# Kernel optimization log

Hardware: AMD Instinct MI355X
Metric: run time of the kernel (lower is better)

## Reference

```python
import jax, jax.numpy as jnp
import numpy as np

B, S, D, H, HD, I = 8, 512, 2048, 32, 64, 8192
REL = 2 * 512 - 1  # 1023
EPS = 1e-6
SCALE = float(np.sqrt(HD))


def _layernorm(x, g, b):
    mu = jnp.mean(x, axis=-1, keepdims=True)
    var = jnp.mean(jnp.square(x - mu), axis=-1, keepdims=True)
    return (x - mu) / jnp.sqrt(var + EPS) * g + b


def setup_inputs() -> dict:
    key = jax.random.key(0)
    ks = jax.random.split(key, 10)
    s = 0.02
    return {
        "hidden_states": jax.random.normal(ks[0], (B, S, D), dtype=jnp.float32),
        "wq": jax.random.normal(ks[1], (D, D), dtype=jnp.float32) * s,
        "wk": jax.random.normal(ks[2], (D, D), dtype=jnp.float32) * s,
        "wv": jax.random.normal(ks[3], (D, D), dtype=jnp.float32) * s,
        "wo": jax.random.normal(ks[4], (D, D), dtype=jnp.float32) * s,
        "rel_pos": jax.random.normal(ks[5], (REL, HD), dtype=jnp.float32),
        "ln1_g": jnp.ones((D,), jnp.float32),
        "ln1_b": jnp.zeros((D,), jnp.float32),
        "gate_w": jax.random.normal(ks[6], (D, I), dtype=jnp.float32) * s,
        "up_w": jax.random.normal(ks[7], (D, I), dtype=jnp.float32) * s,
        "down_w": jax.random.normal(ks[8], (I, D), dtype=jnp.float32) * s,
        "ln2_g": jnp.ones((D,), jnp.float32),
        "ln2_b": jnp.zeros((D,), jnp.float32),
    }


def reference(hidden_states, wq, wk, wv, wo, rel_pos, ln1_g, ln1_b,
              gate_w, up_w, down_w, ln2_g, ln2_b):
    x = hidden_states
    # --- MultiHeadAttentionXL ---
    q = (x @ wq).reshape(B, S, H, HD)
    k = (x @ wk).reshape(B, S, H, HD)
    v = (x @ wv).reshape(B, S, H, HD)
    scores = jnp.einsum('bqhd,bkhd->bhqk', q, k) / SCALE
    # relative position bias (seq_len <= 512 path)
    pos = jnp.arange(S)
    rp = jnp.clip(pos[None, :] - pos[:, None] + 512 - 1, 0, REL - 1)  # [S,S]
    bias = rel_pos[rp].mean(axis=-1)  # [S,S]
    scores = scores + bias[None, None]
    attn = jax.nn.softmax(scores, axis=-1)
    ctx = jnp.einsum('bhqk,bkhd->bqhd', attn, v).reshape(B, S, D)
    attn_out = ctx @ wo
    # residual + post-LN
    h = _layernorm(x + attn_out, ln1_g, ln1_b)
    # --- FeedForwardXL (SwiGLU) ---
    gate = jax.nn.silu(h @ gate_w)
    up = h @ up_w
    ffn = (gate * up) @ down_w
    h = _layernorm(h + ffn, ln2_g, ln2_b)
    return h
```

## Files before the change

kernel.cpp:

```cpp
#include <hip/hip_runtime.h>
#include <cstdint>
#include <cstddef>

typedef _Float16 f16;
typedef _Float16 f16x8 __attribute__((ext_vector_type(8)));
typedef _Float16 f16x4 __attribute__((ext_vector_type(4)));
typedef _Float16 f16x2 __attribute__((ext_vector_type(2)));
typedef float    f32x4 __attribute__((ext_vector_type(4)));

constexpr int S_ = 512, D_ = 2048, H_ = 32, HD_ = 64, I_ = 8192;
constexpr int M_ = 4096;

enum { OP_F32 = 0, OP_F16 = 1, OP_SILU = 2, OP_QKT = 3, OP_PV = 4,
       OP_QKV = 6, OP_UPG = 7, OP_RES = 8 };

__device__ __forceinline__ void gl_lds16(const void* g, void* lds) {
  __builtin_amdgcn_global_load_lds(
      (const __attribute__((address_space(1))) void*)g,
      (__attribute__((address_space(3))) void*)lds, 16, 0, 0);
}

template <int BM, int BN, int WR, int WC, int OP, bool BF32>
__global__ __launch_bounds__(256, 2) void gemm_k(
    const f16* __restrict__ A, int lda,
    const void* __restrict__ Bv, int ldb,
    void* __restrict__ Cp, int ldc,
    int K, int bh0, const float* __restrict__ relmean,
    const void* __restrict__ Bv2, const void* __restrict__ Bv3) {
  constexpr int BK = 32;
  constexpr int WM = BM / WR, WN = BN / WC;
  constexpr int IM = WM / 16, IN = WN / 16;
  constexpr int CA = BM / 64, CB = BN / 64;
  __shared__ __align__(16) f16 As[BM * BK];
  __shared__ __align__(16) f16 Bs[BN * BK];
  const int tid = threadIdx.x, wave = tid >> 6, lane = tid & 63;
  const int wm = wave / WC, wn = wave % WC;
  const int bn = blockIdx.x, bm = blockIdx.y, bz = blockIdx.z;

  long aoff = 0, boff = 0;
  if constexpr (OP == OP_QKT) {
    int bh = bh0 + bz;
    long hb = (long)(bh >> 5) * (S_ * D_) + (long)(bh & (H_ - 1)) * HD_;
    aoff = hb; boff = hb;
  }
  if constexpr (OP == OP_PV) {
    int bh = bh0 + bz;
    aoff = (long)bz * S_ * S_;
    boff = (long)bh * HD_ * S_;
  }

  const f16* Ab = A + aoff + (long)bm * BM * lda;
  const f16* Bb = nullptr;
  const float* Bf = nullptr;
  if constexpr (BF32) {
    const float* base = (const float*)Bv;
    if constexpr (OP == OP_QKV)
      base = (bz == 0) ? (const float*)Bv : (bz == 1) ? (const float*)Bv2
                                                      : (const float*)Bv3;
    Bf = base + (long)bn * BN;
  } else {
    Bb = (const f16*)Bv + boff + (long)bn * BN * ldb;
  }

  f32x4 acc[IM][IN];
#pragma unroll
  for (int i = 0; i < IM; i++)
#pragma unroll
    for (int j = 0; j < IN; j++) acc[i][j] = {0.f, 0.f, 0.f, 0.f};

  const int lr = lane >> 2, l4 = lane & 3;
  const int q8 = (lane >> 4) * 8, l15 = lane & 15;
  constexpr int NG = BN / 4;
  constexpr int KPT = BN / 32;
  const int ng = tid & (NG - 1), kg = tid / NG;

  for (int kt = 0; kt < K; kt += BK) {
#pragma unroll
    for (int c = 0; c < CA; c++) {
      int reg = wave * CA + c;
      int row = reg * 16 + lr;
      gl_lds16(Ab + (long)row * lda + kt + l4 * 8, &As[reg * 512]);
    }
    if constexpr (!BF32) {
#pragma unroll
      for (int c = 0; c < CB; c++) {
        int reg = wave * CB + c;
        int row = reg * 16 + lr;
        gl_lds16(Bb + (long)row * ldb + kt + l4 * 8, &Bs[reg * 512]);
      }
    } else {
      f32x4 v[KPT];
#pragma unroll
      for (int i2 = 0; i2 < KPT; i2++)
        v[i2] = *(const f32x4*)&Bf[(long)(kt + kg * KPT + i2) * ldb + ng * 4];
#pragma unroll
      for (int j2 = 0; j2 < 4; j2++) {
        int n = ng * 4 + j2;
        int k0 = (kg * KPT) ^ ((ng & 3) * 8);
        if constexpr (KPT == 4) {
          f16x4 w = {(f16)v[0][j2], (f16)v[1][j2], (f16)v[2][j2], (f16)v[3][j2]};
          *(f16x4*)&Bs[n * BK + k0] = w;
        } else {
          f16x2 w = {(f16)v[0][j2], (f16)v[1][j2]};
          *(f16x2*)&Bs[n * BK + k0] = w;
        }
      }
    }
    __syncthreads();
    f16x8 af[IM], bfr[IN];
#pragma unroll
    for (int i = 0; i < IM; i++)
      af[i] = *(const f16x8*)&As[(wm * WM + i * 16 + l15) * BK + q8];
#pragma unroll
    for (int j = 0; j < IN; j++) {
      int colL = wn * WN + j * 16 + l15;
      int koff = BF32 ? (q8 ^ (((colL >> 2) & 3) * 8)) : q8;
      bfr[j] = *(const f16x8*)&Bs[colL * BK + koff];
    }
#pragma unroll
    for (int i = 0; i < IM; i++)
#pragma unroll
      for (int j = 0; j < IN; j++)
        acc[i][j] = __builtin_amdgcn_mfma_f32_16x16x32_f16(af[i], bfr[j], acc[i][j], 0, 0, 0);
    __syncthreads();
  }

  const int r0 = bm * BM + wm * WM + (lane >> 4) * 4;
  const int c0 = bn * BN + wn * WN + l15;
#pragma unroll
  for (int i = 0; i < IM; i++) {
#pragma unroll
    for (int j = 0; j < IN; j++) {
      int rowb = r0 + i * 16;
      int col = c0 + j * 16;
      if constexpr (OP == OP_F32) {
        float* C = (float*)Cp;
#pragma unroll
        for (int t = 0; t < 4; t++) C[(long)(rowb + t) * ldc + col] = acc[i][j][t];
      } else if constexpr (OP == OP_F16) {
        f16* C = (f16*)Cp;
#pragma unroll
        for (int t = 0; t < 4; t++) C[(long)(rowb + t) * ldc + col] = (f16)acc[i][j][t];
      } else if constexpr (OP == OP_SILU) {
        f16* C = (f16*)Cp;
#pragma unroll
        for (int t = 0; t < 4; t++) {
          float v = acc[i][j][t];
          C[(long)(rowb + t) * ldc + col] = (f16)(v / (1.f + __expf(-v)));
        }
      } else if constexpr (OP == OP_UPG) {
        f16* C = (f16*)Cp;
        const f16* G = (const f16*)Bv2;
#pragma unroll
        for (int t = 0; t < 4; t++) {
          long idx = (long)(rowb + t) * ldc + col;
          C[idx] = (f16)((float)G[idx] * acc[i][j][t]);
        }
      } else if constexpr (OP == OP_RES) {
        f16* C = (f16*)Cp;
#pragma unroll
        for (int t = 0; t < 4; t++) {
          long idx = (long)(rowb + t) * ldc + col;
          C[idx] = (f16)(acc[i][j][t] + relmean[idx]);
        }
      } else if constexpr (OP == OP_QKT) {
        f16* C = (f16*)Cp + (long)bz * S_ * S_;
#pragma unroll
        for (int t = 0; t < 4; t++) {
          int r = rowb + t;
          C[(long)r * S_ + col] = (f16)(acc[i][j][t] * 0.125f + relmean[col - r + 511]);
        }
      } else if constexpr (OP == OP_PV) {
        int bh = bh0 + bz;
        f16* C = (f16*)Cp + (long)(bh >> 5) * (S_ * D_) + (long)(bh & (H_ - 1)) * HD_;
#pragma unroll
        for (int t = 0; t < 4; t++) C[(long)(rowb + t) * ldc + col] = (f16)acc[i][j][t];
      } else if constexpr (OP == OP_QKV) {
        f16* C = (f16*)Cp;
        if (bz < 2) {
          f16* Cq = C + (long)bz * M_ * D_;
#pragma unroll
          for (int t = 0; t < 4; t++) Cq[(long)(rowb + t) * ldc + col] = (f16)acc[i][j][t];
        } else {
          f16* Cv = C + (long)2 * M_ * D_;
          int b = rowb >> 9, s0 = rowb & 511, h = col >> 6, hd = col & 63;
          f16x4 pk;
#pragma unroll
          for (int t = 0; t < 4; t++) pk[t] = (f16)acc[i][j][t];
          *(f16x4*)&Cv[((long)(b * H_ + h) * HD_ + hd) * S_ + s0] = pk;
        }
      }
    }
  }
}

__global__ void cvt_f16_k(const float* __restrict__ in, f16* __restrict__ out, int n4) {
  int i = blockIdx.x * 256 + threadIdx.x;
  if (i >= n4) return;
  f32x4 v = ((const f32x4*)in)[i];
  f16x4 o;
#pragma unroll
  for (int t = 0; t < 4; t++) o[t] = (f16)v[t];
  ((f16x4*)out)[i] = o;
}

__global__ void relmean_k(const float* __restrict__ rel, float* __restrict__ rm) {
  int i = blockIdx.x * 256 + threadIdx.x;
  if (i >= 1023) return;
  float s = 0.f;
#pragma unroll 8
  for (int d = 0; d < 64; d++) s += rel[i * 64 + d];
  rm[i] = s * (1.f / 64.f);
}

__global__ __launch_bounds__(256) void softmax_k(f16* __restrict__ Sc) {
  int r = blockIdx.x * 4 + (threadIdx.x >> 6);
  int lane = threadIdx.x & 63;
  f16* s = Sc + (long)r * S_;
  f16x8 d = *(const f16x8*)&s[lane * 8];
  float v[8], mx = -1e30f;
#pragma unroll
  for (int i = 0; i < 8; i++) { v[i] = (float)d[i]; mx = fmaxf(mx, v[i]); }
  for (int off = 32; off; off >>= 1) mx = fmaxf(mx, __shfl_xor(mx, off));
  float sum = 0.f;
#pragma unroll
  for (int i = 0; i < 8; i++) { v[i] = __expf(v[i] - mx); sum += v[i]; }
  for (int off = 32; off; off >>= 1) sum += __shfl_xor(sum, off);
  float rs = 1.f / sum;
  f16x8 o;
#pragma unroll
  for (int i = 0; i < 8; i++) o[i] = (f16)(v[i] * rs);
  *(f16x8*)&s[lane * 8] = o;
}

__global__ __launch_bounds__(256) void ln_k(const float* __restrict__ X,
                                            const float* __restrict__ Y,
                                            const float* __restrict__ g,
                                            const float* __restrict__ b,
                                            float* __restrict__ outF,
                                            f16* __restrict__ outH) {
  int row = blockIdx.x;
  const float* x = X + (long)row * D_;
  const float* y = Y + (long)row * D_;
  int t = threadIdx.x;
  float v[8], sum = 0.f, sq = 0.f;
#pragma unroll
  for (int i = 0; i < 8; i++) {
    int idx = t + i * 256;
    float val = x[idx] + y[idx];
    v[i] = val; sum += val; sq += val * val;
  }
  for (int off = 32; off; off >>= 1) { sum += __shfl_down(sum, off); sq += __shfl_down(sq, off); }
  __shared__ float s1[4], s2[4];
  if ((t & 63) == 0) { s1[t >> 6] = sum; s2[t >> 6] = sq; }
  __syncthreads();
  sum = s1[0] + s1[1] + s1[2] + s1[3];
  sq = s2[0] + s2[1] + s2[2] + s2[3];
  float mu = sum * (1.f / D_);
  float rstd = rsqrtf(sq * (1.f / D_) - mu * mu + 1e-6f);
#pragma unroll
  for (int i = 0; i < 8; i++) {
    int idx = t + i * 256;
    float nv = (v[i] - mu) * rstd * g[idx] + b[idx];
    outF[(long)row * D_ + idx] = nv;
    outH[(long)row * D_ + idx] = (f16)nv;
  }
}

__global__ __launch_bounds__(256) void ln2s_k(const f16* __restrict__ X,
                                              const float* __restrict__ g,
                                              const float* __restrict__ b,
                                              float* __restrict__ outF) {
  int row = blockIdx.x;
  const f16* x = X + (long)row * D_;
  int t = threadIdx.x;
  float v[8], sum = 0.f, sq = 0.f;
#pragma unroll
  for (int i = 0; i < 8; i++) {
    float val = (float)x[t + i * 256];
    v[i] = val; sum += val; sq += val * val;
  }
  for (int off = 32; off; off >>= 1) { sum += __shfl_down(sum, off); sq += __shfl_down(sq, off); }
  __shared__ float s1[4], s2[4];
  if ((t & 63) == 0) { s1[t >> 6] = sum; s2[t >> 6] = sq; }
  __syncthreads();
  sum = s1[0] + s1[1] + s1[2] + s1[3];
  sq = s2[0] + s2[1] + s2[2] + s2[3];
  float mu = sum * (1.f / D_);
  float rstd = rsqrtf(sq * (1.f / D_) - mu * mu + 1e-6f);
#pragma unroll
  for (int i = 0; i < 8; i++) {
    int idx = t + i * 256;
    outF[(long)row * D_ + idx] = (v[i] - mu) * rstd * g[idx] + b[idx];
  }
}

extern "C" void kernel_launch(void* const* d_in, const int* in_sizes, int n_in,
                              void* d_out, int out_size, void* d_ws, size_t ws_size,
                              hipStream_t stream) {
  const float* x    = (const float*)d_in[0];
  const float* wq   = (const float*)d_in[1];
  const float* wk   = (const float*)d_in[2];
  const float* wv   = (const float*)d_in[3];
  const float* wo   = (const float*)d_in[4];
  const float* rel  = (const float*)d_in[5];
  const float* ln1g = (const float*)d_in[6];
  const float* ln1b = (const float*)d_in[7];
  const float* gw   = (const float*)d_in[8];
  const float* uw   = (const float*)d_in[9];
  const float* dw   = (const float*)d_in[10];
  const float* ln2g = (const float*)d_in[11];
  const float* ln2b = (const float*)d_in[12];
  float* out = (float*)d_out;

  constexpr size_t MD2 = (size_t)M_ * D_ * 2;
  if (ws_size < 8 * MD2 + 4096) return;
  char* w = (char*)d_ws;
  f16* qb  = (f16*)(w + 0 * MD2);
  f16* vT  = (f16*)(w + 2 * MD2);
  f16* xb  = (f16*)(w + 3 * MD2);
  f16* sc  = (f16*)(w + 4 * MD2);
  f16* h1h = (f16*)(w + 6 * MD2);
  float* relmean = (float*)(w + 8 * MD2);
  f16* ctxb = xb;
  float* attn_out = (float*)qb;
  float* h1 = (float*)sc;
  f16* gc = qb;
  f16* h2h = h1h;

  cvt_f16_k<<<M_ * D_ / 4 / 256, 256, 0, stream>>>(x, xb, M_ * D_ / 4);
  relmean_k<<<4, 256, 0, stream>>>(rel, relmean);

  gemm_k<128, 128, 2, 2, OP_QKV, true><<<dim3(16, 32, 3), 256, 0, stream>>>(
      xb, D_, wq, D_, qb, D_, D_, 0, nullptr, wk, wv);

  for (int c = 0; c < 4; c++) {
    int bh0 = c * 64;
    gemm_k<128, 128, 2, 2, OP_QKT, false><<<dim3(4, 4, 64), 256, 0, stream>>>(
        qb, D_, qb + (size_t)M_ * D_, D_, sc, S_, HD_, bh0, relmean, nullptr, nullptr);
    softmax_k<<<64 * S_ / 4, 256, 0, stream>>>(sc);
    gemm_k<64, 64, 2, 2, OP_PV, false><<<dim3(1, 8, 64), 256, 0, stream>>>(
        sc, S_, vT, S_, ctxb, D_, S_, bh0, nullptr, nullptr, nullptr);
  }

  gemm_k<128, 64, 2, 2, OP_F32, true><<<dim3(32, 32, 1), 256, 0, stream>>>(
      ctxb, D_, wo, D_, attn_out, D_, D_, 0, nullptr, nullptr, nullptr);
  ln_k<<<M_, 256, 0, stream>>>(x, attn_out, ln1g, ln1b, h1, h1h);

  gemm_k<128, 128, 2, 2, OP_SILU, true><<<dim3(64, 32, 1), 256, 0, stream>>>(
      h1h, D_, gw, I_, gc, I_, D_, 0, nullptr, nullptr, nullptr);
  gemm_k<128, 128, 2, 2, OP_UPG, true><<<dim3(64, 32, 1), 256, 0, stream>>>(
      h1h, D_, uw, I_, gc, I_, D_, 0, nullptr, gc, nullptr);
  gemm_k<128, 64, 2, 2, OP_RES, true><<<dim3(32, 32, 1), 256, 0, stream>>>(
      gc, I_, dw, D_, h2h, D_, I_, 0, h1, nullptr, nullptr);
  ln2s_k<<<M_, 256, 0, stream>>>(h2h, ln2g, ln2b, out);
}
```

Baseline: 1.306 ms.

## Pre-transpose weights to f16, fuse gate/up GEMM, split FFN into halves

```diff
diff --git a/kernel.cpp b/kernel.cpp
--- a/kernel.cpp
+++ b/kernel.cpp
@@ -5,14 +5,13 @@
 typedef _Float16 f16;
 typedef _Float16 f16x8 __attribute__((ext_vector_type(8)));
 typedef _Float16 f16x4 __attribute__((ext_vector_type(4)));
-typedef _Float16 f16x2 __attribute__((ext_vector_type(2)));
 typedef float    f32x4 __attribute__((ext_vector_type(4)));
 
 constexpr int S_ = 512, D_ = 2048, H_ = 32, HD_ = 64, I_ = 8192;
 constexpr int M_ = 4096;
-
-enum { OP_F32 = 0, OP_F16 = 1, OP_SILU = 2, OP_QKT = 3, OP_PV = 4,
-       OP_QKV = 6, OP_UPG = 7, OP_RES = 8 };
+constexpr int IH_ = 4096;
+
+enum { OP_F32 = 0, OP_QKT = 3, OP_PV = 4, OP_QKV = 6, OP_GU = 9, OP_ADD = 10 };
 
 __device__ __forceinline__ void gl_lds16(const void* g, void* lds) {
   __builtin_amdgcn_global_load_lds(
@@ -20,19 +19,20 @@
       (__attribute__((address_space(3))) void*)lds, 16, 0, 0);
 }
 
-template <int BM, int BN, int WR, int WC, int OP, bool BF32>
+template <int BM, int BN, int WR, int WC, int OP>
 __global__ __launch_bounds__(256, 2) void gemm_k(
     const f16* __restrict__ A, int lda,
-    const void* __restrict__ Bv, int ldb,
+    const f16* __restrict__ B, int ldb,
     void* __restrict__ Cp, int ldc,
     int K, int bh0, const float* __restrict__ relmean,
-    const void* __restrict__ Bv2, const void* __restrict__ Bv3) {
+    const f16* __restrict__ B2) {
   constexpr int BK = 32;
+  constexpr bool GU = (OP == OP_GU);
   constexpr int WM = BM / WR, WN = BN / WC;
   constexpr int IM = WM / 16, IN = WN / 16;
   constexpr int CA = BM / 64, CB = BN / 64;
   __shared__ __align__(16) f16 As[BM * BK];
-  __shared__ __align__(16) f16 Bs[BN * BK];
+  __shared__ __align__(16) f16 Bs[(GU ? 2 : 1) * BN * BK];
   const int tid = threadIdx.x, wave = tid >> 6, lane = tid & 63;
   const int wm = wave / WC, wn = wave % WC;
   const int bn = blockIdx.x, bm = blockIdx.y, bz = blockIdx.z;
@@ -48,80 +48,58 @@
     aoff = (long)bz * S_ * S_;
     boff = (long)bh * HD_ * S_;
   }
+  if constexpr (OP == OP_QKV) boff = (long)bz * D_ * D_;
 
   const f16* Ab = A + aoff + (long)bm * BM * lda;
-  const f16* Bb = nullptr;
-  const float* Bf = nullptr;
-  if constexpr (BF32) {
-    const float* base = (const float*)Bv;
-    if constexpr (OP == OP_QKV)
-      base = (bz == 0) ? (const float*)Bv : (bz == 1) ? (const float*)Bv2
-                                                      : (const float*)Bv3;
-    Bf = base + (long)bn * BN;
-  } else {
-    Bb = (const f16*)Bv + boff + (long)bn * BN * ldb;
-  }
-
-  f32x4 acc[IM][IN];
+  const f16* Bb = B + boff + (long)bn * BN * ldb;
+  const f16* Bb2 = nullptr;
+  if constexpr (GU) Bb2 = B2 + (long)bn * BN * ldb;
+
+  f32x4 acc[IM][IN], acc2[IM][IN];
 #pragma unroll
   for (int i = 0; i < IM; i++)
 #pragma unroll
-    for (int j = 0; j < IN; j++) acc[i][j] = {0.f, 0.f, 0.f, 0.f};
+    for (int j = 0; j < IN; j++) {
+      acc[i][j] = {0.f, 0.f, 0.f, 0.f};
+      if constexpr (GU) acc2[i][j] = {0.f, 0.f, 0.f, 0.f};
+    }
 
   const int lr = lane >> 2, l4 = lane & 3;
   const int q8 = (lane >> 4) * 8, l15 = lane & 15;
-  constexpr int NG = BN / 4;
-  constexpr int KPT = BN / 32;
-  const int ng = tid & (NG - 1), kg = tid / NG;
 
   for (int kt = 0; kt < K; kt += BK) {
 #pragma unroll
     for (int c = 0; c < CA; c++) {
       int reg = wave * CA + c;
-      int row = reg * 16 + lr;
-      gl_lds16(Ab + (long)row * lda + kt + l4 * 8, &As[reg * 512]);
-    }
-    if constexpr (!BF32) {
-#pragma unroll
-      for (int c = 0; c < CB; c++) {
-        int reg = wave * CB + c;
-        int row = reg * 16 + lr;
-        gl_lds16(Bb + (long)row * ldb + kt + l4 * 8, &Bs[reg * 512]);
-      }
-    } else {
-      f32x4 v[KPT];
-#pragma unroll
-      for (int i2 = 0; i2 < KPT; i2++)
-        v[i2] = *(const f32x4*)&Bf[(long)(kt + kg * KPT + i2) * ldb + ng * 4];
-#pragma unroll
-      for (int j2 = 0; j2 < 4; j2++) {
-        int n = ng * 4 + j2;
-        int k0 = (kg * KPT) ^ ((ng & 3) * 8);
-        if constexpr (KPT == 4) {
-          f16x4 w = {(f16)v[0][j2], (f16)v[1][j2], (f16)v[2][j2], (f16)v[3][j2]};
-          *(f16x4*)&Bs[n * BK + k0] = w;
-        } else {
-          f16x2 w = {(f16)v[0][j2], (f16)v[1][j2]};
-          *(f16x2*)&Bs[n * BK + k0] = w;
-        }
-      }
+      gl_lds16(Ab + (long)(reg * 16 + lr) * lda + kt + l4 * 8, &As[reg * 512]);
+    }
+#pragma unroll
+    for (int c = 0; c < CB; c++) {
+      int reg = wave * CB + c;
+      gl_lds16(Bb + (long)(reg * 16 + lr) * ldb + kt + l4 * 8, &Bs[reg * 512]);
+      if constexpr (GU)
+        gl_lds16(Bb2 + (long)(reg * 16 + lr) * ldb + kt + l4 * 8,
+                 &Bs[BN * BK + reg * 512]);
     }
     __syncthreads();
-    f16x8 af[IM], bfr[IN];
+    f16x8 af[IM], bf[IN], bf2[IN];
 #pragma unroll
     for (int i = 0; i < IM; i++)
       af[i] = *(const f16x8*)&As[(wm * WM + i * 16 + l15) * BK + q8];
 #pragma unroll
     for (int j = 0; j < IN; j++) {
       int colL = wn * WN + j * 16 + l15;
-      int koff = BF32 ? (q8 ^ (((colL >> 2) & 3) * 8)) : q8;
-      bfr[j] = *(const f16x8*)&Bs[colL * BK + koff];
+      bf[j] = *(const f16x8*)&Bs[colL * BK + q8];
+      if constexpr (GU) bf2[j] = *(const f16x8*)&Bs[BN * BK + colL * BK + q8];
     }
 #pragma unroll
     for (int i = 0; i < IM; i++)
 #pragma unroll
-      for (int j = 0; j < IN; j++)
-        acc[i][j] = __builtin_amdgcn_mfma_f32_16x16x32_f16(af[i], bfr[j], acc[i][j], 0, 0, 0);
+      for (int j = 0; j < IN; j++) {
+        acc[i][j] = __builtin_amdgcn_mfma_f32_16x16x32_f16(af[i], bf[j], acc[i][j], 0, 0, 0);
+        if constexpr (GU)
+          acc2[i][j] = __builtin_amdgcn_mfma_f32_16x16x32_f16(af[i], bf2[j], acc2[i][j], 0, 0, 0);
+      }
     __syncthreads();
   }
 
@@ -137,31 +115,16 @@
         float* C = (float*)Cp;
 #pragma unroll
         for (int t = 0; t < 4; t++) C[(long)(rowb + t) * ldc + col] = acc[i][j][t];
-      } else if constexpr (OP == OP_F16) {
+      } else if constexpr (OP == OP_ADD) {
+        float* C = (float*)Cp;
+#pragma unroll
+        for (int t = 0; t < 4; t++) C[(long)(rowb + t) * ldc + col] += acc[i][j][t];
+      } else if constexpr (OP == OP_GU) {
         f16* C = (f16*)Cp;
 #pragma unroll
-        for (int t = 0; t < 4; t++) C[(long)(rowb + t) * ldc + col] = (f16)acc[i][j][t];
-      } else if constexpr (OP == OP_SILU) {
-        f16* C = (f16*)Cp;
-#pragma unroll
         for (int t = 0; t < 4; t++) {
-          float v = acc[i][j][t];
-          C[(long)(rowb + t) * ldc + col] = (f16)(v / (1.f + __expf(-v)));
-        }
-      } else if constexpr (OP == OP_UPG) {
-        f16* C = (f16*)Cp;
-        const f16* G = (const f16*)Bv2;
-#pragma unroll
-        for (int t = 0; t < 4; t++) {
-          long idx = (long)(rowb + t) * ldc + col;
-          C[idx] = (f16)((float)G[idx] * acc[i][j][t]);
-        }
-      } else if constexpr (OP == OP_RES) {
-        f16* C = (f16*)Cp;
-#pragma unroll
-        for (int t = 0; t < 4; t++) {
-          long idx = (long)(rowb + t) * ldc + col;
-          C[idx] = (f16)(acc[i][j][t] + relmean[idx]);
+          float g = acc[i][j][t], u = acc2[i][j][t];
+          C[(long)(rowb + t) * ldc + col] = (f16)(g / (1.f + __expf(-g)) * u);
         }
       } else if constexpr (OP == OP_QKT) {
         f16* C = (f16*)Cp + (long)bz * S_ * S_;
@@ -194,6 +157,33 @@
   }
 }
 
+__global__ __launch_bounds__(256) void transpose_k(
+    const float* __restrict__ in, int ldin, int k0, int n0,
+    f16* __restrict__ out, int ldout) {
+  __shared__ f16 t[64][68];
+  const int kb = blockIdx.x * 64, nb = blockIdx.y * 64;
+  const int tid = threadIdx.x;
+  {
+    const int kr = tid >> 4, nc = (tid & 15) * 4;
+    const float* src = in + (long)(k0 + kb) * ldin + (n0 + nb);
+#pragma unroll
+    for (int i = 0; i < 4; i++) {
+      int k = kr + i * 16;
+      f32x4 v = *(const f32x4*)&src[(long)k * ldin + nc];
+#pragma unroll
+      for (int j = 0; j < 4; j++) t[nc + j][k] = (f16)v[j];
+    }
+  }
+  __syncthreads();
+  {
+    const int n = tid >> 2, kc = (tid & 3) * 16;
+    f16* dst = out + (long)(nb + n) * ldout + (kb + kc);
+#pragma unroll
+    for (int j = 0; j < 4; j++)
+      *(f16x4*)&dst[j * 4] = *(const f16x4*)&t[n][kc + j * 4];
+  }
+}
+
 __global__ void cvt_f16_k(const float* __restrict__ in, f16* __restrict__ out, int n4) {
   int i = blockIdx.x * 256 + threadIdx.x;
   if (i >= n4) return;
@@ -233,12 +223,11 @@
   *(f16x8*)&s[lane * 8] = o;
 }
 
-__global__ __launch_bounds__(256) void ln_k(const float* __restrict__ X,
-                                            const float* __restrict__ Y,
-                                            const float* __restrict__ g,
-                                            const float* __restrict__ b,
-                                            float* __restrict__ outF,
-                                            f16* __restrict__ outH) {
+__global__ __launch_bounds__(256) void ln1_k(const float* __restrict__ X,
+                                             const float* __restrict__ Y,
+                                             const float* __restrict__ g,
+                                             const float* __restrict__ b,
+                                             f16* __restrict__ outH) {
   int row = blockIdx.x;
   const float* x = X + (long)row * D_;
   const float* y = Y + (long)row * D_;
@@ -261,23 +250,24 @@
 #pragma unroll
   for (int i = 0; i < 8; i++) {
     int idx = t + i * 256;
-    float nv = (v[i] - mu) * rstd * g[idx] + b[idx];
-    outF[(long)row * D_ + idx] = nv;
-    outH[(long)row * D_ + idx] = (f16)nv;
-  }
-}
-
-__global__ __launch_bounds__(256) void ln2s_k(const f16* __restrict__ X,
+    outH[(long)row * D_ + idx] = (f16)((v[i] - mu) * rstd * g[idx] + b[idx]);
+  }
+}
+
+__global__ __launch_bounds__(256) void ln2f_k(const float* __restrict__ X,
+                                              const f16* __restrict__ Y,
                                               const float* __restrict__ g,
                                               const float* __restrict__ b,
                                               float* __restrict__ outF) {
   int row = blockIdx.x;
-  const f16* x = X + (long)row * D_;
+  const float* x = X + (long)row * D_;
+  const f16* y = Y + (long)row * D_;
   int t = threadIdx.x;
   float v[8], sum = 0.f, sq = 0.f;
 #pragma unroll
   for (int i = 0; i < 8; i++) {
-    float val = (float)x[t + i * 256];
+    int idx = t + i * 256;
+    float val = x[idx] + (float)y[idx];
     v[i] = val; sum += val; sq += val * val;
   }
   for (int off = 32; off; off >>= 1) { sum += __shfl_down(sum, off); sq += __shfl_down(sq, off); }
@@ -316,42 +306,58 @@
   constexpr size_t MD2 = (size_t)M_ * D_ * 2;
   if (ws_size < 8 * MD2 + 4096) return;
   char* w = (char*)d_ws;
-  f16* qb  = (f16*)(w + 0 * MD2);
-  f16* vT  = (f16*)(w + 2 * MD2);
-  f16* xb  = (f16*)(w + 3 * MD2);
-  f16* sc  = (f16*)(w + 4 * MD2);
-  f16* h1h = (f16*)(w + 6 * MD2);
+  f16* qb   = (f16*)(w + 0 * MD2);
+  f16* vT   = (f16*)(w + 2 * MD2);
+  f16* xb   = (f16*)(w + 3 * MD2);
+  f16* sc   = (f16*)(w + 4 * MD2);
+  f16* h1h  = (f16*)(w + 6 * MD2);
+  f16* s7   = (f16*)(w + 7 * MD2);
   float* relmean = (float*)(w + 8 * MD2);
   f16* ctxb = xb;
   float* attn_out = (float*)qb;
-  float* h1 = (float*)sc;
-  f16* gc = qb;
-  f16* h2h = h1h;
+  f16* wqT  = sc;
+  f16* woT  = s7;
+  f16* gwTh = qb;
+  f16* uwTh = (f16*)(w + 1 * MD2);
+  f16* gch  = vT;
+  f16* dwTh = s7;
+  float* facc = (float*)sc;
 
   cvt_f16_k<<<M_ * D_ / 4 / 256, 256, 0, stream>>>(x, xb, M_ * D_ / 4);
   relmean_k<<<4, 256, 0, stream>>>(rel, relmean);
-
-  gemm_k<128, 128, 2, 2, OP_QKV, true><<<dim3(16, 32, 3), 256, 0, stream>>>(
-      xb, D_, wq, D_, qb, D_, D_, 0, nullptr, wk, wv);
+  transpose_k<<<dim3(32, 32), 256, 0, stream>>>(wq, D_, 0, 0, wqT, D_);
+  transpose_k<<<dim3(32, 32), 256, 0, stream>>>(wk, D_, 0, 0, wqT + (size_t)D_ * D_, D_);
+  transpose_k<<<dim3(32, 32), 256, 0, stream>>>(wv, D_, 0, 0, wqT + 2 * (size_t)D_ * D_, D_);
+  transpose_k<<<dim3(32, 32), 256, 0, stream>>>(wo, D_, 0, 0, woT, D_);
+
+  gemm_k<128, 128, 2, 2, OP_QKV><<<dim3(16, 32, 3), 256, 0, stream>>>(
+      xb, D_, wqT, D_, qb, D_, D_, 0, nullptr, nullptr);
 
   for (int c = 0; c < 4; c++) {
     int bh0 = c * 64;
-    gemm_k<128, 128, 2, 2, OP_QKT, false><<<dim3(4, 4, 64), 256, 0, stream>>>(
-        qb, D_, qb + (size_t)M_ * D_, D_, sc, S_, HD_, bh0, relmean, nullptr, nullptr);
+    gemm_k<128, 128, 2, 2, OP_QKT><<<dim3(4, 4, 64), 256, 0, stream>>>(
+        qb, D_, qb + (size_t)M_ * D_, D_, sc, S_, HD_, bh0, relmean, nullptr);
     softmax_k<<<64 * S_ / 4, 256, 0, stream>>>(sc);
-    gemm_k<64, 64, 2, 2, OP_PV, false><<<dim3(1, 8, 64), 256, 0, stream>>>(
-        sc, S_, vT, S_, ctxb, D_, S_, bh0, nullptr, nullptr, nullptr);
-  }
-
-  gemm_k<128, 64, 2, 2, OP_F32, true><<<dim3(32, 32, 1), 256, 0, stream>>>(
-      ctxb, D_, wo, D_, attn_out, D_, D_, 0, nullptr, nullptr, nullptr);
-  ln_k<<<M_, 256, 0, stream>>>(x, attn_out, ln1g, ln1b, h1, h1h);
-
-  gemm_k<128, 128, 2, 2, OP_SILU, true><<<dim3(64, 32, 1), 256, 0, stream>>>(
-      h1h, D_, gw, I_, gc, I_, D_, 0, nullptr, nullptr, nullptr);
-  gemm_k<128, 128, 2, 2, OP_UPG, true><<<dim3(64, 32, 1), 256, 0, stream>>>(
-      h1h, D_, uw, I_, gc, I_, D_, 0, nullptr, gc, nullptr);
-  gemm_k<128, 64, 2, 2, OP_RES, true><<<dim3(32, 32, 1), 256, 0, stream>>>(
-      gc, I_, dw, D_, h2h, D_, I_, 0, h1, nullptr, nullptr);
-  ln2s_k<<<M_, 256, 0, stream>>>(h2h, ln2g, ln2b, out);
-}
+    gemm_k<64, 64, 2, 2, OP_PV><<<dim3(1, 8, 64), 256, 0, stream>>>(
+        sc, S_, vT, S_, ctxb, D_, S_, bh0, nullptr, nullptr);
+  }
+
+  gemm_k<128, 128, 2, 2, OP_F32><<<dim3(16, 32, 1), 256, 0, stream>>>(
+      ctxb, D_, woT, D_, attn_out, D_, D_, 0, nullptr, nullptr);
+  ln1_k<<<M_, 256, 0, stream>>>(x, attn_out, ln1g, ln1b, h1h);
+
+  for (int h = 0; h < 2; h++) {
+    transpose_k<<<dim3(32, 64), 256, 0, stream>>>(gw, I_, 0, h * IH_, gwTh, D_);
+    transpose_k<<<dim3(32, 64), 256, 0, stream>>>(uw, I_, 0, h * IH_, uwTh, D_);
+    transpose_k<<<dim3(64, 32), 256, 0, stream>>>(dw, D_, h * IH_, 0, dwTh, IH_);
+    gemm_k<128, 64, 2, 2, OP_GU><<<dim3(IH_ / 64, 32, 1), 256, 0, stream>>>(
+        h1h, D_, gwTh, D_, gch, IH_, D_, 0, nullptr, uwTh);
+    if (h == 0)
+      gemm_k<128, 128, 2, 2, OP_F32><<<dim3(16, 32, 1), 256, 0, stream>>>(
+          gch, IH_, dwTh, IH_, facc, D_, IH_, 0, nullptr, nullptr);
+    else
+      gemm_k<128, 128, 2, 2, OP_ADD><<<dim3(16, 32, 1), 256, 0, stream>>>(
+          gch, IH_, dwTh, IH_, facc, D_, IH_, 0, nullptr, nullptr);
+  }
+  ln2f_k<<<M_, 256, 0, stream>>>(facc, h1h, ln2g, ln2b, out);
+}
```

New measurement: 1.249 ms. 1.05x faster.
